# Optimization experiments

Measured on AMD Instinct MI355X. Metric: run time of the kernel, lower is better.

The kernel has to match this reference:

```python
import jax, jax.numpy as jnp
import numpy as np

NUM_DEPTH_BINS = 64
EPS = 1e-8


def bilinear_grid_sample(feats, grid):
    """torch.nn.functional.grid_sample, mode='bilinear', padding_mode='zeros',
    align_corners=False.  feats: [N, C, H, W]; grid: [N, Ho, Wo, 2] in [-1, 1].
    Returns [N, C, Ho, Wo]."""
    N, C, H, W = feats.shape
    x = (grid[..., 0] + 1.0) * (W * 0.5) - 0.5  # [N, Ho, Wo]
    y = (grid[..., 1] + 1.0) * (H * 0.5) - 0.5
    x0 = jnp.floor(x)
    y0 = jnp.floor(y)
    wx1 = x - x0
    wy1 = y - y0
    wx0 = 1.0 - wx1
    wy0 = 1.0 - wy1
    feats_flat = feats.reshape(N, C, H * W)

    def gather(ix, iy):
        valid = (ix >= 0) & (ix <= W - 1) & (iy >= 0) & (iy <= H - 1)
        ixc = jnp.clip(ix, 0, W - 1).astype(jnp.int32)
        iyc = jnp.clip(iy, 0, H - 1).astype(jnp.int32)
        idx = (iyc * W + ixc).reshape(N, 1, -1)  # [N,1,Ho*Wo]
        f = jnp.take_along_axis(feats_flat, idx, axis=2).reshape(N, C, *ix.shape[1:])
        return f * valid[:, None].astype(feats.dtype)

    out = (gather(x0, y0) * (wx0 * wy0)[:, None]
           + gather(x0 + 1, y0) * (wx1 * wy0)[:, None]
           + gather(x0, y0 + 1) * (wx0 * wy1)[:, None]
           + gather(x0 + 1, y0 + 1) * (wx1 * wy1)[:, None])
    return out


def _cost_volume(cur_feats, src_feats, src_extrinsics, src_Ks, cur_invK, min_depth, max_depth):
    B, K, C, H, W = src_feats.shape
    D = NUM_DEPTH_BINS
    # log-spaced depth planes, shape [B, D, 1, 1]
    ramp = jnp.linspace(0.0, 1.0, D).reshape(1, D, 1, 1).astype(cur_feats.dtype)
    depth_planes_bd11 = jnp.exp(jnp.log(min_depth) + jnp.log(max_depth / min_depth) * ramp)
    # BackprojectDepth: half-pixel-centered homogeneous pixel coords [3, N]
    xs, ys = jnp.meshgrid(jnp.arange(W, dtype=cur_feats.dtype) + 0.5,
                          jnp.arange(H, dtype=cur_feats.dtype) + 0.5)
    pix_3n = jnp.stack([xs.ravel(), ys.ravel(), jnp.ones(H * W, cur_feats.dtype)])
    cam_dirs_b3n = jnp.einsum('bij,jn->bin', cur_invK[:, :3, :3], pix_3n)
    world_bd3n = depth_planes_bd11.reshape(B, D, 1, 1) * cam_dirs_b3n[:, None]  # [B,D,3,N]
    world_bd4n = jnp.concatenate(
        [world_bd3n, jnp.ones((B, D, 1, H * W), world_bd3n.dtype)], axis=2)
    # Project3D: P = K @ extrinsics, project, perspective divide
    P_bk34 = jnp.einsum('bkij,bkjl->bkil', src_Ks, src_extrinsics)[:, :, :3]
    cam_bkd3n = jnp.einsum('bkij,bdjn->bkdin', P_bk34, world_bd4n)  # [B,K,D,3,N]
    z_bkdn = cam_bkd3n[:, :, :, 2]
    pix_bkd2n = cam_bkd3n[:, :, :, :2] / (z_bkdn[:, :, :, None] + EPS)
    # uv = 2 * pix * (1/W, 1/H) - 1
    u = 2.0 * pix_bkd2n[:, :, :, 0] / W - 1.0
    v = 2.0 * pix_bkd2n[:, :, :, 1] / H - 1.0
    grid = jnp.stack([u, v], axis=-1).reshape(B * K, D * H, W, 2)
    warped = bilinear_grid_sample(src_feats.reshape(B * K, C, H, W), grid)
    warped = warped.reshape(B, K, C, D, H, W)
    mask = (z_bkdn > 0).astype(cur_feats.dtype).reshape(B, K, D, H, W)
    # channel dot product with current features, masked, summed over views
    dots_bkdhw = jnp.einsum('bkcdhw,bchw->bkdhw', warped, cur_feats) * mask
    cost_volume_bdhw = dots_bkdhw.sum(axis=1)
    return cost_volume_bdhw


def setup_inputs() -> dict:
    key = jax.random.key(0)
    B, K, C, H, W = 1, 7, 16, 96, 128
    k1, k2 = jax.random.split(key)
    cur_feats = jax.random.normal(k1, (B, C, H, W), jnp.float32)
    src_feats = jax.random.normal(k2, (B, K, C, H, W), jnp.float32)
    rng = np.random.default_rng(0)
    fx = 0.8 * W
    Kmat = np.array([[fx, 0, W / 2, 0], [0, fx, H / 2, 0],
                     [0, 0, 1, 0], [0, 0, 0, 1]], np.float32)

    def small_pose():
        aa = rng.normal(size=3) * 0.05
        th = np.linalg.norm(aa)
        ax = aa / (th + 1e-12)
        Kx = np.array([[0, -ax[2], ax[1]], [ax[2], 0, -ax[0]], [-ax[1], ax[0], 0]])
        R = np.eye(3) + np.sin(th) * Kx + (1 - np.cos(th)) * (Kx @ Kx)
        T = np.eye(4, dtype=np.float64)
        T[:3, :3] = R
        T[:3, 3] = rng.normal(size=3) * 0.08
        return T

    src_extrinsics = np.stack([[small_pose() for _ in range(K)] for _ in range(B)])
    src_poses = np.linalg.inv(src_extrinsics)
    return {
        'cur_feats': cur_feats,
        'src_feats': src_feats,
        'src_extrinsics': jnp.asarray(src_extrinsics, jnp.float32),
        'src_poses': jnp.asarray(src_poses, jnp.float32),
        'src_Ks': jnp.asarray(np.broadcast_to(Kmat, (B, K, 4, 4)).copy()),
        'cur_invK': jnp.asarray(np.broadcast_to(np.linalg.inv(Kmat), (B, 4, 4)).astype(np.float32).copy()),
        'min_depth': jnp.full((B, 1, 1, 1), 0.25, jnp.float32),
        'max_depth': jnp.full((B, 1, 1, 1), 5.0, jnp.float32),
    }


def reference(cur_feats, src_feats, src_extrinsics, src_poses, src_Ks, cur_invK, min_depth, max_depth):
    del src_poses  # unused, matching the original (del src_poses)
    return _cost_volume(cur_feats, src_feats, src_extrinsics, src_Ks, cur_invK, min_depth, max_depth)
```

## Files before the change

### kernel.cpp

```cpp
#include <hip/hip_runtime.h>

#define CV_H 96
#define CV_W 128
#define CV_C 16
#define CV_K 7
#define CV_D 64
#define CV_EPS 1e-8f
#define CV_HW (CV_H * CV_W)

typedef _Float16 v2h __attribute__((ext_vector_type(2)));
typedef _Float16 v8h __attribute__((ext_vector_type(8)));

#if __has_builtin(__builtin_amdgcn_fdot2)
#define FDOT2(a, b, c) __builtin_amdgcn_fdot2((a), (b), (c), false)
#else
#define FDOT2(a, b, c) ((float)(a)[0] * (float)(b)[0] + (float)(a)[1] * (float)(b)[1] + (c))
#endif

__global__ __launch_bounds__(256) void cv_prep(
    const float* __restrict__ cur, const float* __restrict__ src,
    const float* __restrict__ extr, const float* __restrict__ Ks,
    const float* __restrict__ invK, const float* __restrict__ minD,
    const float* __restrict__ maxD,
    float* __restrict__ depths, float* __restrict__ M,
    _Float16* __restrict__ srcT, _Float16* __restrict__ curT) {
    if (blockIdx.x == 0) {
        int t = threadIdx.x;
        if (t < CV_D) {
            float mn = minD[0], mx = maxD[0];
            float ramp = (float)t * (1.0f / (CV_D - 1));
            depths[t] = expf(logf(mn) + logf(mx / mn) * ramp);
        }
        if (t < CV_K) {
            const float* Km = Ks + t * 16;
            const float* E  = extr + t * 16;
            float P[3][4];
            for (int i = 0; i < 3; ++i)
                for (int j = 0; j < 4; ++j) {
                    float s = 0.f;
                    for (int l = 0; l < 4; ++l) s += Km[i * 4 + l] * E[l * 4 + j];
                    P[i][j] = s;
                }
            float* Mk = M + t * 12;
            for (int i = 0; i < 3; ++i)
                for (int j = 0; j < 3; ++j) {
                    float s = 0.f;
                    for (int l = 0; l < 3; ++l) s += P[i][l] * invK[l * 4 + j];
                    Mk[i * 3 + j] = s;
                }
            for (int i = 0; i < 3; ++i) Mk[9 + i] = P[i][3];
        }
    }
    int tid = blockIdx.x * 256 + threadIdx.x;
    int c    = tid & (CV_C - 1);
    int rest = tid >> 4;
    int w    = rest & (CV_W - 1);
    int gh   = rest >> 7;
    int h    = gh % CV_H;
    int g    = gh / CV_H;
    if (g < CV_K) {
        srcT[tid] = (_Float16)src[((g * CV_C + c) * CV_H + h) * CV_W + w];
    } else {
        curT[tid - CV_K * CV_HW * CV_C] = (_Float16)cur[(c * CV_H + h) * CV_W + w];
    }
}

__device__ __forceinline__ float dot16h(v8h a0, v8h a1, v8h b0, v8h b1) {
    const v2h* pa0 = (const v2h*)&a0; const v2h* pb0 = (const v2h*)&b0;
    const v2h* pa1 = (const v2h*)&a1; const v2h* pb1 = (const v2h*)&b1;
    float s = 0.f;
#pragma unroll
    for (int i = 0; i < 4; ++i) s = FDOT2(pa0[i], pb0[i], s);
#pragma unroll
    for (int i = 0; i < 4; ++i) s = FDOT2(pa1[i], pb1[i], s);
    return s;
}

__global__ __launch_bounds__(256) void cv_main(
    const _Float16* __restrict__ srcT,
    const _Float16* __restrict__ curT,
    const float* __restrict__ depths,
    const float* __restrict__ Mg,
    float* __restrict__ out) {
    const int bx = blockIdx.x;
    const int wb = bx & 15;
    const int hb = (bx >> 4) % 12;
    const int db = bx / 192;
    const int wx = threadIdx.x & 7;
    const int hy = (threadIdx.x >> 3) & 7;
    const int dd = threadIdx.x >> 6;
    const int w = wb * 8 + wx;
    const int h = hb * 8 + hy;
    const int d = db * 4 + dd;

    const float px = w + 0.5f;
    const float py = h + 0.5f;
    const float depth = depths[d];

    const v8h* cp = (const v8h*)(curT + (h * CV_W + w) * CV_C);
    const v8h c0 = cp[0], c1 = cp[1];

    float acc = 0.f;
#pragma unroll
    for (int k = 0; k < CV_K; ++k) {
        const float* Mk = Mg + k * 12;
        float qx = Mk[0] * px + Mk[1] * py + Mk[2];
        float qy = Mk[3] * px + Mk[4] * py + Mk[5];
        float qz = Mk[6] * px + Mk[7] * py + Mk[8];
        float cx = depth * qx + Mk[9];
        float cy = depth * qy + Mk[10];
        float cz = depth * qz + Mk[11];
        if (cz > 0.f) {
            float inv = 1.0f / (cz + CV_EPS);
            float x = cx * inv - 0.5f;
            float y = cy * inv - 0.5f;
            float xf = floorf(x), yf = floorf(y);
            float wx1 = x - xf, wy1 = y - yf;
            float wx0 = 1.f - wx1, wy0 = 1.f - wy1;
            int x0 = (int)xf, y0 = (int)yf;
            int x1 = x0 + 1, y1 = y0 + 1;
            bool vx0 = (unsigned)x0 < (unsigned)CV_W;
            bool vx1 = (unsigned)x1 < (unsigned)CV_W;
            bool vy0 = (unsigned)y0 < (unsigned)CV_H;
            bool vy1 = (unsigned)y1 < (unsigned)CV_H;
            int cx0 = min(max(x0, 0), CV_W - 1);
            int cx1 = min(max(x1, 0), CV_W - 1);
            int cy0 = min(max(y0, 0), CV_H - 1);
            int cy1 = min(max(y1, 0), CV_H - 1);
            const v8h* base = (const v8h*)srcT + (size_t)k * (CV_HW * 2);
            const v8h* r0 = base + cy0 * (CV_W * 2);
            const v8h* r1 = base + cy1 * (CV_W * 2);
            v8h a00 = r0[cx0 * 2], b00 = r0[cx0 * 2 + 1];
            v8h a10 = r0[cx1 * 2], b10 = r0[cx1 * 2 + 1];
            v8h a01 = r1[cx0 * 2], b01 = r1[cx0 * 2 + 1];
            v8h a11 = r1[cx1 * 2], b11 = r1[cx1 * 2 + 1];
            float w00 = (vx0 && vy0) ? wx0 * wy0 : 0.f;
            float w10 = (vx1 && vy0) ? wx1 * wy0 : 0.f;
            float w01 = (vx0 && vy1) ? wx0 * wy1 : 0.f;
            float w11 = (vx1 && vy1) ? wx1 * wy1 : 0.f;
            acc += w00 * dot16h(a00, b00, c0, c1)
                 + w10 * dot16h(a10, b10, c0, c1)
                 + w01 * dot16h(a01, b01, c0, c1)
                 + w11 * dot16h(a11, b11, c0, c1);
        }
    }
    out[(d * CV_H + h) * CV_W + w] = acc;
}

extern "C" void kernel_launch(void* const* d_in, const int* in_sizes, int n_in,
                              void* d_out, int out_size, void* d_ws, size_t ws_size,
                              hipStream_t stream) {
    const float* cur_feats = (const float*)d_in[0];
    const float* src_feats = (const float*)d_in[1];
    const float* extr      = (const float*)d_in[2];
    const float* Ks        = (const float*)d_in[4];
    const float* invK      = (const float*)d_in[5];
    const float* minD      = (const float*)d_in[6];
    const float* maxD      = (const float*)d_in[7];
    float* out = (float*)d_out;

    float* wsf    = (float*)d_ws;
    float* depths = wsf;
    float* M      = wsf + 64;
    _Float16* srcT = (_Float16*)(wsf + 256);
    _Float16* curT = srcT + CV_K * CV_HW * CV_C;

    int n_total = (CV_K + 1) * CV_C * CV_HW;
    cv_prep<<<n_total / 256, 256, 0, stream>>>(cur_feats, src_feats, extr, Ks,
                                               invK, minD, maxD, depths, M,
                                               srcT, curT);

    cv_main<<<CV_D / 4 * (CV_H / 8) * (CV_W / 8), 256, 0, stream>>>(
        srcT, curT, depths, M, out);
}
```

Baseline: 34.90 us.

## Transpose features through LDS with vector loads and branchless sampling

The prep kernel now handles one feature row per block. It reads float4 values coalesced, transposes them through shared memory, and writes packed 8-half vectors into the channel-last layout, replacing the strided scalar gathers. The main kernel drops the cz>0 branch: it always samples with clamped coordinates and masks the result with a validity factor, which removes divergence but issues loads even for points behind the camera. It also adds a launch-bounds occupancy hint of four blocks.

```diff
diff --git a/kernel.cpp b/kernel.cpp
--- a/kernel.cpp
+++ b/kernel.cpp
@@ -24,7 +24,8 @@
     const float* __restrict__ maxD,
     float* __restrict__ depths, float* __restrict__ M,
     _Float16* __restrict__ srcT, _Float16* __restrict__ curT) {
-    if (blockIdx.x == 0) {
+    const int b = blockIdx.x;
+    if (b == (CV_K + 1) * CV_H) {
         int t = threadIdx.x;
         if (t < CV_D) {
             float mn = minD[0], mx = maxD[0];
@@ -50,19 +51,33 @@
                 }
             for (int i = 0; i < 3; ++i) Mk[9 + i] = P[i][3];
         }
+        return;
     }
-    int tid = blockIdx.x * 256 + threadIdx.x;
-    int c    = tid & (CV_C - 1);
-    int rest = tid >> 4;
-    int w    = rest & (CV_W - 1);
-    int gh   = rest >> 7;
-    int h    = gh % CV_H;
-    int g    = gh / CV_H;
-    if (g < CV_K) {
-        srcT[tid] = (_Float16)src[((g * CV_C + c) * CV_H + h) * CV_W + w];
-    } else {
-        curT[tid - CV_K * CV_HW * CV_C] = (_Float16)cur[(c * CV_H + h) * CV_W + w];
+    const int g = b / CV_H;
+    const int h = b % CV_H;
+    const float* rowBase = (g < CV_K) ? (src + (size_t)g * CV_C * CV_HW + h * CV_W)
+                                      : (cur + h * CV_W);
+    __shared__ float lds[CV_C][CV_W + 2];
+    const int t = threadIdx.x;
+#pragma unroll
+    for (int i = 0; i < 2; ++i) {
+        int f  = t + i * 256;
+        int c  = f >> 5;
+        int w4 = (f & 31) << 2;
+        float4 v = *(const float4*)(rowBase + (size_t)c * CV_HW + w4);
+        lds[c][w4 + 0] = v.x; lds[c][w4 + 1] = v.y;
+        lds[c][w4 + 2] = v.z; lds[c][w4 + 3] = v.w;
     }
+    __syncthreads();
+    const int p  = t >> 1;
+    const int cb = (t & 1) << 3;
+    v8h o;
+#pragma unroll
+    for (int j = 0; j < 8; ++j) o[j] = (_Float16)lds[cb + j][p];
+    _Float16* dst = (g < CV_K)
+        ? (srcT + ((size_t)g * CV_HW + h * CV_W + p) * CV_C + cb)
+        : (curT + ((size_t)h * CV_W + p) * CV_C + cb);
+    *(v8h*)dst = o;
 }
 
 __device__ __forceinline__ float dot16h(v8h a0, v8h a1, v8h b0, v8h b1) {
@@ -76,7 +91,7 @@
     return s;
 }
 
-__global__ __launch_bounds__(256) void cv_main(
+__global__ __launch_bounds__(256, 4) void cv_main(
     const _Float16* __restrict__ srcT,
     const _Float16* __restrict__ curT,
     const float* __restrict__ depths,
@@ -110,39 +125,39 @@
         float cx = depth * qx + Mk[9];
         float cy = depth * qy + Mk[10];
         float cz = depth * qz + Mk[11];
-        if (cz > 0.f) {
-            float inv = 1.0f / (cz + CV_EPS);
-            float x = cx * inv - 0.5f;
-            float y = cy * inv - 0.5f;
-            float xf = floorf(x), yf = floorf(y);
-            float wx1 = x - xf, wy1 = y - yf;
-            float wx0 = 1.f - wx1, wy0 = 1.f - wy1;
-            int x0 = (int)xf, y0 = (int)yf;
-            int x1 = x0 + 1, y1 = y0 + 1;
-            bool vx0 = (unsigned)x0 < (unsigned)CV_W;
-            bool vx1 = (unsigned)x1 < (unsigned)CV_W;
-            bool vy0 = (unsigned)y0 < (unsigned)CV_H;
-            bool vy1 = (unsigned)y1 < (unsigned)CV_H;
-            int cx0 = min(max(x0, 0), CV_W - 1);
-            int cx1 = min(max(x1, 0), CV_W - 1);
-            int cy0 = min(max(y0, 0), CV_H - 1);
-            int cy1 = min(max(y1, 0), CV_H - 1);
-            const v8h* base = (const v8h*)srcT + (size_t)k * (CV_HW * 2);
-            const v8h* r0 = base + cy0 * (CV_W * 2);
-            const v8h* r1 = base + cy1 * (CV_W * 2);
-            v8h a00 = r0[cx0 * 2], b00 = r0[cx0 * 2 + 1];
-            v8h a10 = r0[cx1 * 2], b10 = r0[cx1 * 2 + 1];
-            v8h a01 = r1[cx0 * 2], b01 = r1[cx0 * 2 + 1];
-            v8h a11 = r1[cx1 * 2], b11 = r1[cx1 * 2 + 1];
-            float w00 = (vx0 && vy0) ? wx0 * wy0 : 0.f;
-            float w10 = (vx1 && vy0) ? wx1 * wy0 : 0.f;
-            float w01 = (vx0 && vy1) ? wx0 * wy1 : 0.f;
-            float w11 = (vx1 && vy1) ? wx1 * wy1 : 0.f;
-            acc += w00 * dot16h(a00, b00, c0, c1)
-                 + w10 * dot16h(a10, b10, c0, c1)
-                 + w01 * dot16h(a01, b01, c0, c1)
-                 + w11 * dot16h(a11, b11, c0, c1);
-        }
+        float valid = (cz > 0.f) ? 1.f : 0.f;
+        float inv = 1.0f / (fabsf(cz) + CV_EPS);
+        float x = fminf(fmaxf(cx * inv - 0.5f, -4.0f), (float)(CV_W + 3));
+        float y = fminf(fmaxf(cy * inv - 0.5f, -4.0f), (float)(CV_H + 3));
+        float xf = floorf(x), yf = floorf(y);
+        float wx1 = x - xf, wy1 = y - yf;
+        float wx0 = 1.f - wx1, wy0 = 1.f - wy1;
+        int x0 = (int)xf, y0 = (int)yf;
+        int x1 = x0 + 1, y1 = y0 + 1;
+        bool vx0 = (unsigned)x0 < (unsigned)CV_W;
+        bool vx1 = (unsigned)x1 < (unsigned)CV_W;
+        bool vy0 = (unsigned)y0 < (unsigned)CV_H;
+        bool vy1 = (unsigned)y1 < (unsigned)CV_H;
+        int cx0 = min(max(x0, 0), CV_W - 1);
+        int cx1 = min(max(x1, 0), CV_W - 1);
+        int cy0 = min(max(y0, 0), CV_H - 1);
+        int cy1 = min(max(y1, 0), CV_H - 1);
+        const v8h* base = (const v8h*)srcT + (size_t)k * (CV_HW * 2);
+        const v8h* r0 = base + cy0 * (CV_W * 2);
+        const v8h* r1 = base + cy1 * (CV_W * 2);
+        v8h a00 = r0[cx0 * 2], b00 = r0[cx0 * 2 + 1];
+        v8h a10 = r0[cx1 * 2], b10 = r0[cx1 * 2 + 1];
+        v8h a01 = r1[cx0 * 2], b01 = r1[cx0 * 2 + 1];
+        v8h a11 = r1[cx1 * 2], b11 = r1[cx1 * 2 + 1];
+        float w00 = (vx0 && vy0) ? wx0 * wy0 : 0.f;
+        float w10 = (vx1 && vy0) ? wx1 * wy0 : 0.f;
+        float w01 = (vx0 && vy1) ? wx0 * wy1 : 0.f;
+        float w11 = (vx1 && vy1) ? wx1 * wy1 : 0.f;
+        float s = w00 * dot16h(a00, b00, c0, c1)
+                + w10 * dot16h(a10, b10, c0, c1)
+                + w01 * dot16h(a01, b01, c0, c1)
+                + w11 * dot16h(a11, b11, c0, c1);
+        acc = fmaf(valid, s, acc);
     }
     out[(d * CV_H + h) * CV_W + w] = acc;
 }
@@ -165,10 +180,8 @@
     _Float16* srcT = (_Float16*)(wsf + 256);
     _Float16* curT = srcT + CV_K * CV_HW * CV_C;
 
-    int n_total = (CV_K + 1) * CV_C * CV_HW;
-    cv_prep<<<n_total / 256, 256, 0, stream>>>(cur_feats, src_feats, extr, Ks,
-                                               invK, minD, maxD, depths, M,
-                                               srcT, curT);
+    cv_prep<<<(CV_K + 1) * CV_H + 1, 256, 0, stream>>>(
+        cur_feats, src_feats, extr, Ks, invK, minD, maxD, depths, M, srcT, curT);
 
     cv_main<<<CV_D / 4 * (CV_H / 8) * (CV_W / 8), 256, 0, stream>>>(
         srcT, curT, depths, M, out);
```

New measurement: 34.30 us. No clear change (-1.7%).
